# Kernel tuning notes

Hardware: AMD Instinct MI355X
Metric: run time of the kernel (lower is better)

The kernel has to match this reference:

```python
import jax, jax.numpy as jnp
import numpy as np

DECAY = 0.9


def setup_inputs() -> dict:
    key = jax.random.key(0)
    k1, k2, k3 = jax.random.split(key, 3)
    B, S, D, M = 4, 4096, 1024, 4096
    x = jax.random.normal(k1, (B, S, D), dtype=jnp.float32)
    w1 = jax.random.normal(k2, (M, D), dtype=jnp.float32) * (1.0 / np.sqrt(D))
    w2 = jax.random.normal(k3, (D, M), dtype=jnp.float32) * (1.0 / np.sqrt(M))
    return {"x": x, "w1": w1, "w2": w2}


def reference(x, w1, w2):
    B, S, D = x.shape
    idx = jnp.arange(S)
    diff = idx[:, None] - idx[None, :]          # [S, S]
    mask = diff >= 0
    # clamp negative exponents before pow to avoid inf, then mask
    d = jnp.where(mask, diff, 0).astype(x.dtype)
    decay_matrix = (DECAY ** d) * (1.0 - DECAY) * mask.astype(x.dtype)  # [S, S]
    # causal exponential-decay EMA as dense matmul: current[b,t] = sum_s dm[t,s] x[b,s]
    current_states = jnp.einsum('ts,bsd->btd', decay_matrix, x)
    # roll by 1 with zeroed first step
    previous_states = jnp.concatenate(
        [jnp.zeros_like(current_states[:, :1]), current_states[:, :-1]], axis=1)
    # MemoryMLP: w2(silu(w1(prev)))
    h = jax.nn.silu(jnp.einsum('btd,md->btm', previous_states, w1))
    mem_out = jnp.einsum('btm,dm->btd', h, w2)
    final_state = current_states[:, -1, :]
    surprise_loss = jnp.mean((mem_out - jax.lax.stop_gradient(x)) ** 2)
    return mem_out, surprise_loss, final_state
```

## Files before the change

kernel.cpp:

```cpp
#include <hip/hip_runtime.h>
#include <hip/hip_bf16.h>
#include <stdint.h>

#define BSZ 4
#define SEQ 4096
#define DIM 1024
#define MDIM 4096
#define DECAYF 0.9f
#define OMD 0.1f
#define CHUNK 128
#define NCHUNK 32
#define DECAY_CHUNK 1.3901844577868923e-06f

typedef __bf16 bf16_t;
typedef __bf16 bf16x8 __attribute__((ext_vector_type(8)));
typedef __bf16 bf16x4 __attribute__((ext_vector_type(4)));
typedef float floatx4 __attribute__((ext_vector_type(4)));

__device__ __forceinline__ void load16_lds(const void* g, void* l) {
  __builtin_amdgcn_global_load_lds(
      (__attribute__((address_space(1))) void*)g,
      (__attribute__((address_space(3))) void*)l,
      16, 0, 0);
}

__global__ void scan_chunk_kernel(const float* __restrict__ x,
                                  float* __restrict__ chunk_end) {
  int t = blockIdx.x * 256 + threadIdx.x;
  int d = t & (DIM - 1);
  int c = (t >> 10) & (NCHUNK - 1);
  int b = t >> 15;
  const float* xp = x + ((size_t)(b * SEQ + c * CHUNK + 64)) * DIM + d;
  float p = 0.f;
#pragma unroll 8
  for (int s = 0; s < 64; ++s) p = DECAYF * p + OMD * xp[(size_t)s * DIM];
  chunk_end[t] = p;
}

__global__ void scan_carry_kernel(const float* __restrict__ chunk_end,
                                  float* __restrict__ carry_in,
                                  float* __restrict__ final_state) {
  int t = blockIdx.x * 256 + threadIdx.x;
  int d = t & (DIM - 1);
  int b = t >> 10;
  float carry = 0.f;
#pragma unroll
  for (int c = 0; c < NCHUNK; ++c) {
    int idx = (b * NCHUNK + c) * DIM + d;
    carry_in[idx] = carry;
    carry = carry * DECAY_CHUNK + chunk_end[idx];
  }
  final_state[t] = carry;
}

__global__ void scan_emit_kernel(const float* __restrict__ x,
                                 const float* __restrict__ carry_in,
                                 bf16_t* __restrict__ prev) {
  int t = blockIdx.x * 256 + threadIdx.x;
  int d = t & (DIM - 1);
  int c = (t >> 10) & (NCHUNK - 1);
  int b = t >> 15;
  size_t base = ((size_t)(b * SEQ + c * CHUNK)) * DIM + d;
  const float* xp = x + base;
  bf16_t* pp = prev + base;
  float cs = carry_in[t];
#pragma unroll 4
  for (int s = 0; s < CHUNK; ++s) {
    pp[(size_t)s * DIM] = (bf16_t)cs;
    cs = DECAYF * cs + OMD * xp[(size_t)s * DIM];
  }
}

__global__ void cvt_bf16_kernel(const float* __restrict__ w, bf16_t* __restrict__ o) {
  int t = blockIdx.x * 256 + threadIdx.x;
  float4 v = ((const float4*)w)[t];
  bf16x4 r = { (bf16_t)v.x, (bf16_t)v.y, (bf16_t)v.z, (bf16_t)v.w };
  ((bf16x4*)o)[t] = r;
}

template <int N, int K, int MT, int EPI>
__global__ __launch_bounds__(256) void gemm_bt_kernel(
    const bf16_t* __restrict__ A, const bf16_t* __restrict__ B,
    void* __restrict__ Cout, const float* __restrict__ X,
    float* __restrict__ loss_acc) {
  constexpr int NT = N / 128;
  __shared__ __attribute__((aligned(16))) bf16_t sA0[128 * 64];
  __shared__ __attribute__((aligned(16))) bf16_t sB0[128 * 64];
  __shared__ __attribute__((aligned(16))) bf16_t sA1[128 * 64];
  __shared__ __attribute__((aligned(16))) bf16_t sB1[128 * 64];

  const int tid = threadIdx.x;
  const int wave = tid >> 6;
  const int lane = tid & 63;
  const int bid = blockIdx.x;
  const int xcd = bid & 7;
  const int slot = bid >> 3;
  const int tm = (xcd * (MT / 8) + slot / NT) * 128;
  const int tn = (slot % NT) * 128;
  const int lrow = lane >> 3;
  const int lcol = ((lane & 7) ^ lrow) * 8;
  const int wm = (wave & 1) * 64;
  const int wn = (wave >> 1) * 64;

  floatx4 acc[4][4];
#pragma unroll
  for (int i = 0; i < 4; ++i)
#pragma unroll
    for (int j = 0; j < 4; ++j) acc[i][j] = (floatx4){0.f, 0.f, 0.f, 0.f};

  auto stage = [&](int kt2, bf16_t* bufA, bf16_t* bufB) {
#pragma unroll
    for (int j = 0; j < 4; ++j) {
      const int g = j * 4 + wave;
      load16_lds(A + (size_t)(tm + g * 8 + lrow) * K + kt2 + lcol,
                 (char*)bufA + g * 1024);
      load16_lds(B + (size_t)(tn + g * 8 + lrow) * K + kt2 + lcol,
                 (char*)bufB + g * 1024);
    }
  };

  auto computeHalf = [&](const bf16_t* bufA, const bf16_t* bufB) {
#pragma unroll
    for (int ks = 0; ks < 2; ++ks) {
      const int pchunk = (((ks * 4) + (lane >> 4)) ^ (lane & 7)) * 8;
      bf16x8 af[4], bfr[4];
#pragma unroll
      for (int i = 0; i < 4; ++i)
        af[i] = *(const bf16x8*)&bufA[(size_t)(wm + i * 16 + (lane & 15)) * 64 + pchunk];
#pragma unroll
      for (int j = 0; j < 4; ++j)
        bfr[j] = *(const bf16x8*)&bufB[(size_t)(wn + j * 16 + (lane & 15)) * 64 + pchunk];
#pragma unroll
      for (int i = 0; i < 4; ++i)
#pragma unroll
        for (int j = 0; j < 4; ++j)
          acc[i][j] = __builtin_amdgcn_mfma_f32_16x16x32_bf16(af[i], bfr[j],
                                                              acc[i][j], 0, 0, 0);
    }
  };

  stage(0, sA0, sB0);
#pragma unroll 1
  for (int kt = 0; kt < K; kt += 128) {
    __syncthreads();
    if (kt + 64 < K) stage(kt + 64, sA1, sB1);
    computeHalf(sA0, sB0);
    __syncthreads();
    if (kt + 128 < K) stage(kt + 128, sA0, sB0);
    computeHalf(sA1, sB1);
  }

  const int r0 = (lane >> 4) * 4;
  const int cn = lane & 15;
  if constexpr (EPI == 0) {
    bf16_t* H = (bf16_t*)Cout;
#pragma unroll
    for (int i = 0; i < 4; ++i)
#pragma unroll
      for (int j = 0; j < 4; ++j)
#pragma unroll
        for (int r = 0; r < 4; ++r) {
          int m = tm + wm + i * 16 + r0 + r;
          int n = tn + wn + j * 16 + cn;
          float v = acc[i][j][r];
          v = v / (1.f + __expf(-v));
          H[(size_t)m * N + n] = (bf16_t)v;
        }
  } else {
    float* O = (float*)Cout;
    float ls = 0.f;
#pragma unroll
    for (int i = 0; i < 4; ++i)
#pragma unroll
      for (int j = 0; j < 4; ++j)
#pragma unroll
        for (int r = 0; r < 4; ++r) {
          int m = tm + wm + i * 16 + r0 + r;
          int n = tn + wn + j * 16 + cn;
          size_t off = (size_t)m * N + n;
          float v = acc[i][j][r];
          O[off] = v;
          float dd = v - X[off];
          ls += dd * dd;
        }
#pragma unroll
    for (int s = 32; s > 0; s >>= 1) ls += __shfl_down(ls, s, 64);
    if (lane == 0) atomicAdd(loss_acc, ls);
  }
}

__global__ void finalize_loss_kernel(const float* __restrict__ loss_acc,
                                     float* __restrict__ out) {
  if (threadIdx.x == 0)
    out[0] = loss_acc[0] * (1.0f / (float)(BSZ * SEQ * DIM));
}

extern "C" void kernel_launch(void* const* d_in, const int* in_sizes, int n_in,
                              void* d_out, int out_size, void* d_ws, size_t ws_size,
                              hipStream_t stream) {
  const float* x  = (const float*)d_in[0];
  const float* w1 = (const float*)d_in[1];
  const float* w2 = (const float*)d_in[2];
  float* out = (float*)d_out;

  const int BT = BSZ * SEQ;
  char* ws = (char*)d_ws;
  bf16_t* prev      = (bf16_t*)(ws);
  bf16_t* h         = (bf16_t*)(ws + 33554432ull);
  bf16_t* w1b       = (bf16_t*)(ws + 167772160ull);
  bf16_t* w2b       = (bf16_t*)(ws + 176160768ull);
  float*  chunk_end = (float*)(ws + 184549376ull);
  float*  carry_in  = (float*)(ws + 185073664ull);
  float*  loss_acc  = (float*)(ws + 185597952ull);

  hipMemsetAsync(loss_acc, 0, sizeof(float), stream);

  cvt_bf16_kernel<<<4096, 256, 0, stream>>>(w1, w1b);
  cvt_bf16_kernel<<<4096, 256, 0, stream>>>(w2, w2b);

  scan_chunk_kernel<<<(BSZ * NCHUNK * DIM) / 256, 256, 0, stream>>>(x, chunk_end);
  scan_carry_kernel<<<(BSZ * DIM) / 256, 256, 0, stream>>>(chunk_end, carry_in,
                                                           out + 16777217);
  scan_emit_kernel<<<(BSZ * NCHUNK * DIM) / 256, 256, 0, stream>>>(x, carry_in, prev);

  gemm_bt_kernel<MDIM, DIM, BT / 128, 0>
      <<<(BT / 128) * (MDIM / 128), 256, 0, stream>>>(prev, w1b, h, nullptr, nullptr);

  gemm_bt_kernel<DIM, MDIM, BT / 128, 1>
      <<<(BT / 128) * (DIM / 128), 256, 0, stream>>>(h, w2b, out, x, loss_acc);

  finalize_loss_kernel<<<1, 64, 0, stream>>>(loss_acc, out + 16777216);
}
```

Baseline: 506.7 us.

## Rewrite GEMMs as 256x256-tile 8-wave kernels with interleaved LDS staging

```diff
diff --git a/kernel.cpp b/kernel.cpp
--- a/kernel.cpp
+++ b/kernel.cpp
@@ -23,6 +23,13 @@
       (__attribute__((address_space(3))) void*)l,
       16, 0, 0);
 }
+
+#define BARRIER_MEM()              \
+  do {                             \
+    asm volatile("" ::: "memory"); \
+    __builtin_amdgcn_s_barrier();  \
+    asm volatile("" ::: "memory"); \
+  } while (0)
 
 __global__ void scan_chunk_kernel(const float* __restrict__ x,
                                   float* __restrict__ chunk_end) {
@@ -78,16 +85,40 @@
   ((bf16x4*)o)[t] = r;
 }
 
+#define READ_A(dst, CA, MH)                                                    \
+  _Pragma("unroll") for (int i_ = 0; i_ < 4; ++i_)                             \
+      _Pragma("unroll") for (int k_ = 0; k_ < 2; ++k_)                         \
+          dst[i_][k_] = *(const bf16x8*)((const char*)(CA) + wrBase +          \
+                                         (MH) * 8192 + i_ * 2048 + rbase +     \
+                                         ((k_ * 64 + kc) ^ lswz));
+
+#define READ_B(dst, CB, NH)                                                    \
+  _Pragma("unroll") for (int j_ = 0; j_ < 2; ++j_)                             \
+      _Pragma("unroll") for (int k_ = 0; k_ < 2; ++k_)                         \
+          dst[j_][k_] = *(const bf16x8*)((const char*)(CB) + wcBase +          \
+                                         (NH) * 4096 + j_ * 2048 + rbase +     \
+                                         ((k_ * 64 + kc) ^ lswz));
+
+#define MMQ(AF, BF, MO, NO)                                                    \
+  _Pragma("unroll") for (int k_ = 0; k_ < 2; ++k_)                             \
+      _Pragma("unroll") for (int i_ = 0; i_ < 4; ++i_)                         \
+          _Pragma("unroll") for (int j_ = 0; j_ < 2; ++j_)                     \
+              acc[(MO) + i_][(NO) + j_] =                                      \
+                  __builtin_amdgcn_mfma_f32_16x16x32_bf16(                     \
+                      AF[i_][k_], BF[j_][k_], acc[(MO) + i_][(NO) + j_],       \
+                      0, 0, 0);
+
 template <int N, int K, int MT, int EPI>
-__global__ __launch_bounds__(256) void gemm_bt_kernel(
+__global__ __launch_bounds__(512, 2) void gemm256_kernel(
     const bf16_t* __restrict__ A, const bf16_t* __restrict__ B,
     void* __restrict__ Cout, const float* __restrict__ X,
     float* __restrict__ loss_acc) {
-  constexpr int NT = N / 128;
-  __shared__ __attribute__((aligned(16))) bf16_t sA0[128 * 64];
-  __shared__ __attribute__((aligned(16))) bf16_t sB0[128 * 64];
-  __shared__ __attribute__((aligned(16))) bf16_t sA1[128 * 64];
-  __shared__ __attribute__((aligned(16))) bf16_t sB1[128 * 64];
+  constexpr int NT = N / 256;
+  constexpr int NTK = K / 64;
+  static_assert((NTK & 1) == 0 && NTK >= 4, "even K-tile count");
+  static_assert(MT % 8 == 0, "m-tiles divisible by XCD count");
+  __shared__ __attribute__((aligned(16))) bf16_t sA[2][16384];
+  __shared__ __attribute__((aligned(16))) bf16_t sB[2][16384];
 
   const int tid = threadIdx.x;
   const int wave = tid >> 6;
@@ -95,59 +126,85 @@
   const int bid = blockIdx.x;
   const int xcd = bid & 7;
   const int slot = bid >> 3;
-  const int tm = (xcd * (MT / 8) + slot / NT) * 128;
-  const int tn = (slot % NT) * 128;
-  const int lrow = lane >> 3;
-  const int lcol = ((lane & 7) ^ lrow) * 8;
-  const int wm = (wave & 1) * 64;
-  const int wn = (wave >> 1) * 64;
-
-  floatx4 acc[4][4];
-#pragma unroll
-  for (int i = 0; i < 4; ++i)
+  const int tm = (xcd * (MT / 8) + slot / NT) * 256;
+  const int tn = (slot % NT) * 256;
+  const int wr = wave >> 2;
+  const int wc = wave & 3;
+  const int wrBase = wr * 16384;
+  const int wcBase = wc * 8192;
+  const int rbase = (lane & 15) * 128;
+  const int kc = (lane >> 4) * 16;
+  const int lswz = ((lane >> 1) & 7) << 4;
+  const int srow = wave * 8 + (lane >> 3);
+  const int scolb = ((lane & 7) * 16) ^ (((srow >> 1) & 7) << 4);
+
+  floatx4 acc[8][4];
+#pragma unroll
+  for (int i = 0; i < 8; ++i)
 #pragma unroll
     for (int j = 0; j < 4; ++j) acc[i][j] = (floatx4){0.f, 0.f, 0.f, 0.f};
 
-  auto stage = [&](int kt2, bf16_t* bufA, bf16_t* bufB) {
-#pragma unroll
-    for (int j = 0; j < 4; ++j) {
-      const int g = j * 4 + wave;
-      load16_lds(A + (size_t)(tm + g * 8 + lrow) * K + kt2 + lcol,
-                 (char*)bufA + g * 1024);
-      load16_lds(B + (size_t)(tn + g * 8 + lrow) * K + kt2 + lcol,
-                 (char*)bufB + g * 1024);
+  auto stage_ht = [&](const bf16_t* G, int tb, bf16_t* lbuf, int kt, int h) {
+    char* lbase = (char*)lbuf + h * 16384 + wave * 1024;
+    const char* gbase =
+        (const char*)G + ((size_t)(tb + h * 128 + srow) * K + kt) * 2 + scolb;
+    load16_lds(gbase, lbase);
+    load16_lds(gbase + (size_t)64 * K * 2, lbase + 8192);
+  };
+
+  auto tile4 = [&](int t, bf16_t* cA, bf16_t* cB, bf16_t* nB) {
+    bf16x8 a0[4][2], a1[4][2], b0[2][2], b1[2][2];
+    const int kt2 = (t + 2) * 64;
+    READ_A(a0, cA, 0);
+    READ_B(b0, cB, 0);
+    if (t + 1 < NTK) stage_ht(B, tn, nB, (t + 1) * 64, 1);
+    BARRIER_MEM();
+    __builtin_amdgcn_s_setprio(1);
+    MMQ(a0, b0, 0, 0);
+    __builtin_amdgcn_s_setprio(0);
+    BARRIER_MEM();
+    READ_A(a1, cA, 1);
+    BARRIER_MEM();
+    __builtin_amdgcn_s_setprio(1);
+    MMQ(a1, b0, 4, 0);
+    __builtin_amdgcn_s_setprio(0);
+    BARRIER_MEM();
+    READ_B(b1, cB, 1);
+    if (t + 2 < NTK) {
+      stage_ht(A, tm, cA, kt2, 0);
+      stage_ht(A, tm, cA, kt2, 1);
     }
+    BARRIER_MEM();
+    __builtin_amdgcn_s_setprio(1);
+    MMQ(a1, b1, 4, 2);
+    __builtin_amdgcn_s_setprio(0);
+    BARRIER_MEM();
+    if (t + 2 < NTK) stage_ht(B, tn, cB, kt2, 0);
+    BARRIER_MEM();
+    __builtin_amdgcn_s_setprio(1);
+    MMQ(a0, b1, 0, 2);
+    __builtin_amdgcn_s_setprio(0);
+    if (t + 1 < NTK) {
+      if (t + 2 < NTK) asm volatile("s_waitcnt vmcnt(6)" ::: "memory");
+      else             asm volatile("s_waitcnt vmcnt(0)" ::: "memory");
+    }
+    BARRIER_MEM();
   };
 
-  auto computeHalf = [&](const bf16_t* bufA, const bf16_t* bufB) {
-#pragma unroll
-    for (int ks = 0; ks < 2; ++ks) {
-      const int pchunk = (((ks * 4) + (lane >> 4)) ^ (lane & 7)) * 8;
-      bf16x8 af[4], bfr[4];
-#pragma unroll
-      for (int i = 0; i < 4; ++i)
-        af[i] = *(const bf16x8*)&bufA[(size_t)(wm + i * 16 + (lane & 15)) * 64 + pchunk];
-#pragma unroll
-      for (int j = 0; j < 4; ++j)
-        bfr[j] = *(const bf16x8*)&bufB[(size_t)(wn + j * 16 + (lane & 15)) * 64 + pchunk];
-#pragma unroll
-      for (int i = 0; i < 4; ++i)
-#pragma unroll
-        for (int j = 0; j < 4; ++j)
-          acc[i][j] = __builtin_amdgcn_mfma_f32_16x16x32_bf16(af[i], bfr[j],
-                                                              acc[i][j], 0, 0, 0);
-    }
-  };
-
-  stage(0, sA0, sB0);
+  stage_ht(A, tm, sA[0], 0, 0);
+  stage_ht(A, tm, sA[0], 0, 1);
+  stage_ht(B, tn, sB[0], 0, 0);
+  stage_ht(B, tn, sB[0], 0, 1);
+  stage_ht(A, tm, sA[1], 64, 0);
+  stage_ht(A, tm, sA[1], 64, 1);
+  stage_ht(B, tn, sB[1], 64, 0);
+  asm volatile("s_waitcnt vmcnt(6)" ::: "memory");
+  BARRIER_MEM();
+
 #pragma unroll 1
-  for (int kt = 0; kt < K; kt += 128) {
-    __syncthreads();
-    if (kt + 64 < K) stage(kt + 64, sA1, sB1);
-    computeHalf(sA0, sB0);
-    __syncthreads();
-    if (kt + 128 < K) stage(kt + 128, sA0, sB0);
-    computeHalf(sA1, sB1);
+  for (int t = 0; t < NTK; t += 2) {
+    tile4(t, sA[0], sB[0], sB[1]);
+    tile4(t + 1, sA[1], sB[1], sB[0]);
   }
 
   const int r0 = (lane >> 4) * 4;
@@ -155,13 +212,13 @@
   if constexpr (EPI == 0) {
     bf16_t* H = (bf16_t*)Cout;
 #pragma unroll
-    for (int i = 0; i < 4; ++i)
+    for (int i = 0; i < 8; ++i)
 #pragma unroll
       for (int j = 0; j < 4; ++j)
 #pragma unroll
         for (int r = 0; r < 4; ++r) {
-          int m = tm + wm + i * 16 + r0 + r;
-          int n = tn + wn + j * 16 + cn;
+          int m = tm + wr * 128 + i * 16 + r0 + r;
+          int n = tn + wc * 64 + j * 16 + cn;
           float v = acc[i][j][r];
           v = v / (1.f + __expf(-v));
           H[(size_t)m * N + n] = (bf16_t)v;
@@ -170,13 +227,13 @@
     float* O = (float*)Cout;
     float ls = 0.f;
 #pragma unroll
-    for (int i = 0; i < 4; ++i)
+    for (int i = 0; i < 8; ++i)
 #pragma unroll
       for (int j = 0; j < 4; ++j)
 #pragma unroll
         for (int r = 0; r < 4; ++r) {
-          int m = tm + wm + i * 16 + r0 + r;
-          int n = tn + wn + j * 16 + cn;
+          int m = tm + wr * 128 + i * 16 + r0 + r;
+          int n = tn + wc * 64 + j * 16 + cn;
           size_t off = (size_t)m * N + n;
           float v = acc[i][j][r];
           O[off] = v;
@@ -188,6 +245,10 @@
     if (lane == 0) atomicAdd(loss_acc, ls);
   }
 }
+
+#undef READ_A
+#undef READ_B
+#undef MMQ
 
 __global__ void finalize_loss_kernel(const float* __restrict__ loss_acc,
                                      float* __restrict__ out) {
@@ -223,11 +284,11 @@
                                                            out + 16777217);
   scan_emit_kernel<<<(BSZ * NCHUNK * DIM) / 256, 256, 0, stream>>>(x, carry_in, prev);
 
-  gemm_bt_kernel<MDIM, DIM, BT / 128, 0>
-      <<<(BT / 128) * (MDIM / 128), 256, 0, stream>>>(prev, w1b, h, nullptr, nullptr);
-
-  gemm_bt_kernel<DIM, MDIM, BT / 128, 1>
-      <<<(BT / 128) * (DIM / 128), 256, 0, stream>>>(h, w2b, out, x, loss_acc);
+  gemm256_kernel<MDIM, DIM, BT / 256, 0>
+      <<<(BT / 256) * (MDIM / 256), 512, 0, stream>>>(prev, w1b, h, nullptr, nullptr);
+
+  gemm256_kernel<DIM, MDIM, BT / 256, 1>
+      <<<(BT / 256) * (DIM / 256), 512, 0, stream>>>(h, w2b, out, x, loss_acc);
 
   finalize_loss_kernel<<<1, 64, 0, stream>>>(loss_acc, out + 16777216);
 }
```

Result: faster. 467.5 us (-7.7%).
